# Kernel tuning notes

Hardware: AMD Instinct MI355X
Metric: run time of the kernel (lower is better)

Reference implementation:

```python
import jax, jax.numpy as jnp
import numpy as np

EMBED_DIM = 1024


def setup_inputs() -> dict:
    key = jax.random.key(0)
    ks = jax.random.split(key, 9)
    d = EMBED_DIM
    s = 1.0 / np.sqrt(d)
    x = jax.random.normal(ks[0], (4, 2048, d), dtype=jnp.float32)
    # nn.Linear weights are [out, in]; we store them transposed for x @ W
    Wq = jax.random.uniform(ks[1], (d, d), jnp.float32, -s, s)
    bq = jax.random.uniform(ks[2], (d,), jnp.float32, -s, s)
    Wk = jax.random.uniform(ks[3], (d, d), jnp.float32, -s, s)
    bk = jax.random.uniform(ks[4], (d,), jnp.float32, -s, s)
    Wv = jax.random.uniform(ks[5], (d, d), jnp.float32, -s, s)
    bv = jax.random.uniform(ks[6], (d,), jnp.float32, -s, s)
    Wo = jax.random.uniform(ks[7], (d, d), jnp.float32, -s, s)
    bo = jax.random.uniform(ks[8], (d,), jnp.float32, -s, s)
    return {"x": x, "Wq": Wq, "bq": bq, "Wk": Wk, "bk": bk,
            "Wv": Wv, "bv": bv, "Wo": Wo, "bo": bo}


def reference(x, Wq, bq, Wk, bk, Wv, bv, Wo, bo):
    b, seq_len, d = x.shape
    scaling = 1.0 / jnp.sqrt(jnp.float32(d))
    q = x @ Wq + bq  # [b, s, d]
    k = x @ Wk + bk
    v = x @ Wv + bv
    scores = jnp.einsum('bqd,bkd->bqk', q, k) * scaling  # [b, s, s]
    causal = jnp.tril(jnp.ones((seq_len, seq_len), dtype=bool))
    scores = jnp.where(causal, scores, -jnp.inf)
    attn = jax.nn.softmax(scores, axis=-1)
    out = jnp.einsum('bqk,bkd->bqd', attn, v)
    return out @ Wo + bo
```

## Files before the change

### kernel.cpp

```cpp
#include <hip/hip_runtime.h>
#include <stdint.h>

typedef __bf16 bf16_t;
typedef __bf16 bf16x8 __attribute__((ext_vector_type(8)));
typedef __bf16 bf16x4 __attribute__((ext_vector_type(4)));
typedef float  f32x4  __attribute__((ext_vector_type(4)));

#define DEV __device__ __forceinline__

constexpr int S = 2048, D = 1024, BATCH = 4, MF = BATCH * S;

DEV void gload16(const void* g, void* l) {
  __builtin_amdgcn_global_load_lds(
      (const __attribute__((address_space(1))) void*)g,
      (__attribute__((address_space(3))) void*)(uint32_t)(uintptr_t)l,
      16, 0, 0);
}

template<int EP>
DEV void gemm_body(int tm, int tn, int bz,
                   const bf16_t* __restrict__ A, const bf16_t* __restrict__ B,
                   void* __restrict__ C0, void* __restrict__ C1,
                   void* __restrict__ C2, const float* __restrict__ aux,
                   float* __restrict__ part, int K, int kmax,
                   bf16_t* ldsA, bf16_t* ldsB)
{
  const int m0 = tm * 128, n0 = tn * 128;
  const int tid  = threadIdx.x;
  const int lane = tid & 63;
  const int wave = tid >> 6;
  const int wm = wave & 1, wn = wave >> 1;
  const int l8r = lane >> 3;
  const int swz = ((lane & 7) ^ (lane >> 3)) * 8;
  const int cl  = lane & 15;
  const int qd  = lane >> 4;
  const int ch0 = ((qd ^ (cl & 7)) * 8);

  f32x4 acc[4][4] = {};

  for (int k0 = 0; k0 < kmax; k0 += 64) {
    #pragma unroll
    for (int t = 0; t < 4; ++t) {
      const int rb = wave * 4 + t;
      gload16(A + (long)(m0 + rb * 8 + l8r) * K + (k0 + swz), &ldsA[rb * 512]);
      gload16(B + (long)(n0 + rb * 8 + l8r) * K + (k0 + swz), &ldsB[rb * 512]);
    }
    __syncthreads();
    #pragma unroll
    for (int kk = 0; kk < 64; kk += 32) {
      bf16x8 af[4], bg[4];
      #pragma unroll
      for (int i = 0; i < 4; ++i)
        af[i] = *(const bf16x8*)&ldsA[(wm * 64 + i * 16 + cl) * 64 + (ch0 ^ kk)];
      #pragma unroll
      for (int j = 0; j < 4; ++j)
        bg[j] = *(const bf16x8*)&ldsB[(wn * 64 + j * 16 + cl) * 64 + (ch0 ^ kk)];
      #pragma unroll
      for (int i = 0; i < 4; ++i)
        #pragma unroll
        for (int j = 0; j < 4; ++j)
          acc[i][j] = __builtin_amdgcn_mfma_f32_16x16x32_bf16(af[i], bg[j], acc[i][j], 0, 0, 0);
    }
    __syncthreads();
  }

  #pragma unroll
  for (int i = 0; i < 4; ++i) {
    const int gm0 = m0 + wm * 64 + i * 16 + qd * 4;

    if (EP == 0) {
      float* Co = (float*)C0;
      #pragma unroll
      for (int j = 0; j < 4; ++j) {
        const int gn = n0 + wn * 64 + j * 16 + cl;
        const float bn = aux[gn];
        #pragma unroll
        for (int r = 0; r < 4; ++r)
          Co[(long)(gm0 + r) * D + gn] = acc[i][j][r] + bn;
      }
    }

    if (EP == 1) {
      bf16_t* q  = (bf16_t*)C0;
      bf16_t* k  = (bf16_t*)C1;
      bf16_t* vT = (bf16_t*)C2;
      #pragma unroll
      for (int j = 0; j < 4; ++j) {
        const int gn  = n0 + wn * 64 + j * 16 + cl;
        const int sec = gn >> 10, ln = gn & 1023;
        const float bn = aux[gn];
        if (sec == 2) {
          const int z = gm0 >> 11, s0 = gm0 & 2047;
          bf16x4 v4;
          #pragma unroll
          for (int r = 0; r < 4; ++r) v4[r] = (bf16_t)(acc[i][j][r] + bn);
          *(bf16x4*)&vT[((long)z * D + ln) * S + s0] = v4;
        } else {
          bf16_t* dst = (sec == 0) ? q : k;
          #pragma unroll
          for (int r = 0; r < 4; ++r)
            dst[(long)(gm0 + r) * D + ln] = (bf16_t)(acc[i][j][r] + bn);
        }
      }
    }

    if (EP == 2) {
      bf16_t* probs = (bf16_t*)C0 + (long)bz * S * S;
      float ls[4] = {0.f, 0.f, 0.f, 0.f};
      #pragma unroll
      for (int j = 0; j < 4; ++j) {
        const int gn = n0 + wn * 64 + j * 16 + cl;
        #pragma unroll
        for (int r = 0; r < 4; ++r) {
          const int gm = gm0 + r;
          const float e = (gn <= gm) ? __expf(acc[i][j][r] * 0.03125f) : 0.0f;
          probs[(long)gm * S + gn] = (bf16_t)e;
          ls[r] += e;
        }
      }
      #pragma unroll
      for (int r = 0; r < 4; ++r) {
        float v = ls[r];
        v += __shfl_xor(v, 1); v += __shfl_xor(v, 2);
        v += __shfl_xor(v, 4); v += __shfl_xor(v, 8);
        if (cl == 0)
          part[((long)bz * S + (gm0 + r)) * 32 + tn * 2 + wn] = v;
      }
    }

    if (EP == 3) {
      bf16_t* attn = (bf16_t*)C0 + (long)bz * S * D;
      const float* invl = aux + (long)bz * S;
      float scl[4];
      #pragma unroll
      for (int r = 0; r < 4; ++r) scl[r] = invl[gm0 + r];
      #pragma unroll
      for (int j = 0; j < 4; ++j) {
        const int gn = n0 + wn * 64 + j * 16 + cl;
        #pragma unroll
        for (int r = 0; r < 4; ++r)
          attn[(long)(gm0 + r) * D + gn] = (bf16_t)(acc[i][j][r] * scl[r]);
      }
    }
  }
}

__global__ __launch_bounds__(256, 4) void gemm_qkv(
    const bf16_t* __restrict__ A, const bf16_t* __restrict__ B,
    bf16_t* q, bf16_t* k, bf16_t* vT, const float* __restrict__ bias)
{
  __shared__ __align__(16) bf16_t lA[128 * 64], lB[128 * 64];
  #pragma unroll
  for (int t = 0; t < 2; ++t) {
    const int l = (int)blockIdx.x + t * 768;
    gemm_body<1>(l & 63, l >> 6, 0, A, B, q, k, vT, bias, nullptr,
                 1024, 1024, lA, lB);
  }
}

__global__ __launch_bounds__(256, 4) void gemm_sc(
    const bf16_t* __restrict__ q, const bf16_t* __restrict__ k,
    bf16_t* probs, float* part)
{
  __shared__ __align__(16) bf16_t lA[128 * 64], lB[128 * 64];
  const int l = blockIdx.x, xcd = l & 7, idx = l >> 3;
  const int bz = xcd >> 1;
  const int t  = (xcd & 1) * 68 + idx;
  int tm = (int)((sqrtf(8.0f * t + 1.0f) - 1.0f) * 0.5f);
  while ((tm + 1) * (tm + 2) / 2 <= t) ++tm;
  while (tm * (tm + 1) / 2 > t) --tm;
  const int tn = t - tm * (tm + 1) / 2;
  gemm_body<2>(tm, tn, bz, q + (long)bz * S * D, k + (long)bz * S * D,
               probs, nullptr, nullptr, nullptr, part, 1024, 1024, lA, lB);
}

__global__ __launch_bounds__(256, 4) void gemm_pv(
    const bf16_t* __restrict__ probs, const bf16_t* __restrict__ vT,
    bf16_t* attn, const float* __restrict__ invl)
{
  __shared__ __align__(16) bf16_t lA[128 * 64], lB[128 * 64];
  const int l = blockIdx.x, xcd = l & 7, idx = l >> 3;
  const int bz = xcd >> 1, half = xcd & 1;
  const int slot = idx >> 3, tn = idx & 7;
  const int tm = (slot & 1) ? (slot - 1 + half) : (15 - half - slot);
  const int kmax = (tm + 1) * 128;
  gemm_body<3>(tm, tn, bz, probs + (long)bz * S * S, vT + (long)bz * D * S,
               attn, nullptr, nullptr, invl, nullptr, 2048, kmax, lA, lB);
}

__global__ __launch_bounds__(256, 4) void gemm_oproj(
    const bf16_t* __restrict__ attn, const bf16_t* __restrict__ WoT,
    float* out, const float* __restrict__ bo)
{
  __shared__ __align__(16) bf16_t lA[128 * 64], lB[128 * 64];
  gemm_body<0>(blockIdx.x, blockIdx.y, 0, attn, WoT, out, nullptr, nullptr,
               bo, nullptr, 1024, 1024, lA, lB);
}

__global__ __launch_bounds__(256) void reduce_invl(
    const float* __restrict__ part, float* __restrict__ invl)
{
  const int r = blockIdx.x * 256 + threadIdx.x;
  const int row = r & (S - 1);
  const int cnt = ((row >> 7) + 1) * 2;
  const float* p = part + (long)r * 32;
  float s = 0.f;
  for (int j = 0; j < cnt; ++j) s += p[j];
  invl[r] = 1.0f / s;
}

__global__ __launch_bounds__(256) void cvt_x(
    const float4* __restrict__ in, bf16x4* __restrict__ out, int n4)
{
  const int i = blockIdx.x * 256 + threadIdx.x;
  if (i >= n4) return;
  float4 f = in[i];
  bf16x4 o;
  o.x = (__bf16)f.x; o.y = (__bf16)f.y; o.z = (__bf16)f.z; o.w = (__bf16)f.w;
  out[i] = o;
}

__global__ __launch_bounds__(256) void cvt_w_t4(
    const float* __restrict__ W0, const float* __restrict__ W1,
    const float* __restrict__ W2, const float* __restrict__ W3,
    bf16_t* __restrict__ dst)
{
  const float* W = (blockIdx.z == 0) ? W0 : (blockIdx.z == 1) ? W1
                 : (blockIdx.z == 2) ? W2 : W3;
  bf16_t* WT = dst + (size_t)blockIdx.z * D * D;
  __shared__ float t[32][33];
  const int bx = blockIdx.x, by = blockIdx.y;
  const int tx = threadIdx.x & 31, ty = threadIdx.x >> 5;
  #pragma unroll
  for (int dy = 0; dy < 32; dy += 8)
    t[ty + dy][tx] = W[(long)(by * 32 + ty + dy) * 1024 + bx * 32 + tx];
  __syncthreads();
  #pragma unroll
  for (int dy = 0; dy < 32; dy += 8)
    WT[(long)(bx * 32 + ty + dy) * 1024 + by * 32 + tx] = (bf16_t)t[tx][ty + dy];
}

__global__ __launch_bounds__(256) void stack_bias(
    const float* __restrict__ bq, const float* __restrict__ bk,
    const float* __restrict__ bv, float* __restrict__ o)
{
  const int i = blockIdx.x * 256 + threadIdx.x;
  const float* s = (i < 1024) ? bq : (i < 2048) ? bk : bv;
  o[i] = s[i & 1023];
}

extern "C" void kernel_launch(void* const* d_in, const int* in_sizes, int n_in,
                              void* d_out, int out_size, void* d_ws, size_t ws_size,
                              hipStream_t stream) {
  const float* x  = (const float*)d_in[0];
  const float* Wq = (const float*)d_in[1];
  const float* bq = (const float*)d_in[2];
  const float* Wk = (const float*)d_in[3];
  const float* bk = (const float*)d_in[4];
  const float* Wv = (const float*)d_in[5];
  const float* bv = (const float*)d_in[6];
  const float* Wo = (const float*)d_in[7];
  const float* bo = (const float*)d_in[8];
  float* out = (float*)d_out;

  size_t off = 0;
  auto alloc = [&](size_t bytes) -> void* {
    void* p = (char*)d_ws + off;
    off += (bytes + 255) & ~(size_t)255;
    return p;
  };
  bf16_t* x_b   = (bf16_t*)alloc((size_t)MF * D * 2);
  bf16_t* Wall  = (bf16_t*)alloc((size_t)4 * D * D * 2);
  float*  bqkv  = (float*) alloc((size_t)3 * D * 4);
  bf16_t* q_b   = (bf16_t*)alloc((size_t)MF * D * 2);
  bf16_t* k_b   = (bf16_t*)alloc((size_t)MF * D * 2);
  bf16_t* vT_b  = (bf16_t*)alloc((size_t)BATCH * D * S * 2);
  bf16_t* probs = (bf16_t*)alloc((size_t)BATCH * S * S * 2);
  float*  part  = (float*) alloc((size_t)MF * 32 * 4);
  float*  invl  = (float*) alloc((size_t)MF * 4);
  bf16_t* attn  = (bf16_t*)alloc((size_t)MF * D * 2);
  bf16_t* WqkvT = Wall;
  bf16_t* WoT   = Wall + (size_t)3 * D * D;

  cvt_x<<<dim3((MF * D / 4 + 255) / 256), 256, 0, stream>>>(
      (const float4*)x, (bf16x4*)x_b, MF * D / 4);
  cvt_w_t4<<<dim3(32, 32, 4), 256, 0, stream>>>(Wq, Wk, Wv, Wo, Wall);
  stack_bias<<<dim3(12), 256, 0, stream>>>(bq, bk, bv, bqkv);

  gemm_qkv<<<dim3(768), 256, 0, stream>>>(x_b, WqkvT, q_b, k_b, vT_b, bqkv);

  gemm_sc<<<dim3(544), 256, 0, stream>>>(q_b, k_b, probs, part);

  reduce_invl<<<dim3(MF / 256), 256, 0, stream>>>(part, invl);

  gemm_pv<<<dim3(512), 256, 0, stream>>>(probs, vT_b, attn, invl);

  gemm_oproj<<<dim3(64, 8), 256, 0, stream>>>(attn, WoT, out, bo);
}
```

Measured before the change: 251.7 us.

## Fold output projection into value weights to drop separate O-proj GEMM

Precomputes Wv·Wo as a fused bf16 weight (a small 1024x1024 GEMM) and folds the V bias through Wo, so the QKV GEMM directly produces V·Wo. The PV GEMM then writes the final fp32 output with the softmax normalisation and bias, which removes the full-size output-projection GEMM and the attn intermediate buffer. The cost is an extra weight-product GEMM and a serial per-column dot product for the bias. The weight product is rounded to bf16, which slightly changes numerics. The QKV launch also moves from a persistent two-tile loop to a 2D grid.

```diff
diff --git a/kernel.cpp b/kernel.cpp
--- a/kernel.cpp
+++ b/kernel.cpp
@@ -68,22 +68,10 @@
   for (int i = 0; i < 4; ++i) {
     const int gm0 = m0 + wm * 64 + i * 16 + qd * 4;
 
-    if (EP == 0) {
-      float* Co = (float*)C0;
-      #pragma unroll
-      for (int j = 0; j < 4; ++j) {
-        const int gn = n0 + wn * 64 + j * 16 + cl;
-        const float bn = aux[gn];
-        #pragma unroll
-        for (int r = 0; r < 4; ++r)
-          Co[(long)(gm0 + r) * D + gn] = acc[i][j][r] + bn;
-      }
-    }
-
     if (EP == 1) {
       bf16_t* q  = (bf16_t*)C0;
       bf16_t* k  = (bf16_t*)C1;
-      bf16_t* vT = (bf16_t*)C2;
+      bf16_t* vwT = (bf16_t*)C2;
       #pragma unroll
       for (int j = 0; j < 4; ++j) {
         const int gn  = n0 + wn * 64 + j * 16 + cl;
@@ -94,7 +82,7 @@
           bf16x4 v4;
           #pragma unroll
           for (int r = 0; r < 4; ++r) v4[r] = (bf16_t)(acc[i][j][r] + bn);
-          *(bf16x4*)&vT[((long)z * D + ln) * S + s0] = v4;
+          *(bf16x4*)&vwT[((long)z * D + ln) * S + s0] = v4;
         } else {
           bf16_t* dst = (sec == 0) ? q : k;
           #pragma unroll
@@ -129,17 +117,30 @@
     }
 
     if (EP == 3) {
-      bf16_t* attn = (bf16_t*)C0 + (long)bz * S * D;
+      float* out = (float*)C0 + (long)bz * S * D;
       const float* invl = aux + (long)bz * S;
+      const float* bo = (const float*)C1;
       float scl[4];
       #pragma unroll
       for (int r = 0; r < 4; ++r) scl[r] = invl[gm0 + r];
+      #pragma unroll
+      for (int j = 0; j < 4; ++j) {
+        const int gn = n0 + wn * 64 + j * 16 + cl;
+        const float bn = bo[gn];
+        #pragma unroll
+        for (int r = 0; r < 4; ++r)
+          out[(long)(gm0 + r) * D + gn] = acc[i][j][r] * scl[r] + bn;
+      }
+    }
+
+    if (EP == 4) {
+      bf16_t* Co = (bf16_t*)C0;
       #pragma unroll
       for (int j = 0; j < 4; ++j) {
         const int gn = n0 + wn * 64 + j * 16 + cl;
         #pragma unroll
         for (int r = 0; r < 4; ++r)
-          attn[(long)(gm0 + r) * D + gn] = (bf16_t)(acc[i][j][r] * scl[r]);
+          Co[(long)(gm0 + r) * D + gn] = (bf16_t)acc[i][j][r];
       }
     }
   }
@@ -147,15 +148,11 @@
 
 __global__ __launch_bounds__(256, 4) void gemm_qkv(
     const bf16_t* __restrict__ A, const bf16_t* __restrict__ B,
-    bf16_t* q, bf16_t* k, bf16_t* vT, const float* __restrict__ bias)
+    bf16_t* q, bf16_t* k, bf16_t* vwT, const float* __restrict__ bias)
 {
   __shared__ __align__(16) bf16_t lA[128 * 64], lB[128 * 64];
-  #pragma unroll
-  for (int t = 0; t < 2; ++t) {
-    const int l = (int)blockIdx.x + t * 768;
-    gemm_body<1>(l & 63, l >> 6, 0, A, B, q, k, vT, bias, nullptr,
-                 1024, 1024, lA, lB);
-  }
+  gemm_body<1>(blockIdx.x, blockIdx.y, 0, A, B, q, k, vwT, bias, nullptr,
+               1024, 1024, lA, lB);
 }
 
 __global__ __launch_bounds__(256, 4) void gemm_sc(
@@ -174,9 +171,9 @@
                probs, nullptr, nullptr, nullptr, part, 1024, 1024, lA, lB);
 }
 
-__global__ __launch_bounds__(256, 4) void gemm_pv(
-    const bf16_t* __restrict__ probs, const bf16_t* __restrict__ vT,
-    bf16_t* attn, const float* __restrict__ invl)
+__global__ __launch_bounds__(256, 4) void gemm_pv_out(
+    const bf16_t* __restrict__ probs, const bf16_t* __restrict__ vwT,
+    float* out, const float* __restrict__ invl, const float* __restrict__ bo)
 {
   __shared__ __align__(16) bf16_t lA[128 * 64], lB[128 * 64];
   const int l = blockIdx.x, xcd = l & 7, idx = l >> 3;
@@ -184,17 +181,17 @@
   const int slot = idx >> 3, tn = idx & 7;
   const int tm = (slot & 1) ? (slot - 1 + half) : (15 - half - slot);
   const int kmax = (tm + 1) * 128;
-  gemm_body<3>(tm, tn, bz, probs + (long)bz * S * S, vT + (long)bz * D * S,
-               attn, nullptr, nullptr, invl, nullptr, 2048, kmax, lA, lB);
-}
-
-__global__ __launch_bounds__(256, 4) void gemm_oproj(
-    const bf16_t* __restrict__ attn, const bf16_t* __restrict__ WoT,
-    float* out, const float* __restrict__ bo)
+  gemm_body<3>(tm, tn, bz, probs + (long)bz * S * S, vwT + (long)bz * D * S,
+               out, (void*)bo, nullptr, invl, nullptr, 2048, kmax, lA, lB);
+}
+
+__global__ __launch_bounds__(256, 4) void gemm_wvo(
+    const bf16_t* __restrict__ WoT, const bf16_t* __restrict__ WvN,
+    bf16_t* WvoT)
 {
   __shared__ __align__(16) bf16_t lA[128 * 64], lB[128 * 64];
-  gemm_body<0>(blockIdx.x, blockIdx.y, 0, attn, WoT, out, nullptr, nullptr,
-               bo, nullptr, 1024, 1024, lA, lB);
+  gemm_body<4>(blockIdx.x, blockIdx.y, 0, WoT, WvN, WvoT, nullptr, nullptr,
+               nullptr, nullptr, 1024, 1024, lA, lB);
 }
 
 __global__ __launch_bounds__(256) void reduce_invl(
@@ -225,12 +222,23 @@
     const float* __restrict__ W2, const float* __restrict__ W3,
     bf16_t* __restrict__ dst)
 {
+  const int zmap[4] = {0, 1, 3, 4};
   const float* W = (blockIdx.z == 0) ? W0 : (blockIdx.z == 1) ? W1
                  : (blockIdx.z == 2) ? W2 : W3;
-  bf16_t* WT = dst + (size_t)blockIdx.z * D * D;
-  __shared__ float t[32][33];
+  bf16_t* WT = dst + (size_t)zmap[blockIdx.z] * D * D;
   const int bx = blockIdx.x, by = blockIdx.y;
   const int tx = threadIdx.x & 31, ty = threadIdx.x >> 5;
+
+  if (blockIdx.z == 2) {
+    #pragma unroll
+    for (int dy = 0; dy < 32; dy += 8) {
+      const long idx = (long)(by * 32 + ty + dy) * 1024 + bx * 32 + tx;
+      WT[idx] = (bf16_t)W[idx];
+    }
+    return;
+  }
+
+  __shared__ float t[32][33];
   #pragma unroll
   for (int dy = 0; dy < 32; dy += 8)
     t[ty + dy][tx] = W[(long)(by * 32 + ty + dy) * 1024 + bx * 32 + tx];
@@ -242,11 +250,18 @@
 
 __global__ __launch_bounds__(256) void stack_bias(
     const float* __restrict__ bq, const float* __restrict__ bk,
-    const float* __restrict__ bv, float* __restrict__ o)
+    const float* __restrict__ bv, const float* __restrict__ Wo,
+    float* __restrict__ o)
 {
   const int i = blockIdx.x * 256 + threadIdx.x;
-  const float* s = (i < 1024) ? bq : (i < 2048) ? bk : bv;
-  o[i] = s[i & 1023];
+  if (i < 2048) {
+    o[i] = (i < 1024) ? bq[i] : bk[i & 1023];
+  } else {
+    const int c = i - 2048;
+    float s = 0.f;
+    for (int e = 0; e < 1024; ++e) s += bv[e] * Wo[e * 1024 + c];
+    o[i] = s;
+  }
 }
 
 extern "C" void kernel_launch(void* const* d_in, const int* in_sizes, int n_in,
@@ -270,30 +285,31 @@
     return p;
   };
   bf16_t* x_b   = (bf16_t*)alloc((size_t)MF * D * 2);
-  bf16_t* Wall  = (bf16_t*)alloc((size_t)4 * D * D * 2);
+  bf16_t* Wall  = (bf16_t*)alloc((size_t)5 * D * D * 2);
   float*  bqkv  = (float*) alloc((size_t)3 * D * 4);
   bf16_t* q_b   = (bf16_t*)alloc((size_t)MF * D * 2);
   bf16_t* k_b   = (bf16_t*)alloc((size_t)MF * D * 2);
-  bf16_t* vT_b  = (bf16_t*)alloc((size_t)BATCH * D * S * 2);
+  bf16_t* vwT_b = (bf16_t*)alloc((size_t)BATCH * D * S * 2);
   bf16_t* probs = (bf16_t*)alloc((size_t)BATCH * S * S * 2);
   float*  part  = (float*) alloc((size_t)MF * 32 * 4);
   float*  invl  = (float*) alloc((size_t)MF * 4);
-  bf16_t* attn  = (bf16_t*)alloc((size_t)MF * D * 2);
   bf16_t* WqkvT = Wall;
-  bf16_t* WoT   = Wall + (size_t)3 * D * D;
+  bf16_t* WvoT  = Wall + (size_t)2 * D * D;
+  bf16_t* WvN   = Wall + (size_t)3 * D * D;
+  bf16_t* WoT   = Wall + (size_t)4 * D * D;
 
   cvt_x<<<dim3((MF * D / 4 + 255) / 256), 256, 0, stream>>>(
       (const float4*)x, (bf16x4*)x_b, MF * D / 4);
   cvt_w_t4<<<dim3(32, 32, 4), 256, 0, stream>>>(Wq, Wk, Wv, Wo, Wall);
-  stack_bias<<<dim3(12), 256, 0, stream>>>(bq, bk, bv, bqkv);
-
-  gemm_qkv<<<dim3(768), 256, 0, stream>>>(x_b, WqkvT, q_b, k_b, vT_b, bqkv);
+  stack_bias<<<dim3(12), 256, 0, stream>>>(bq, bk, bv, Wo, bqkv);
+
+  gemm_wvo<<<dim3(8, 8), 256, 0, stream>>>(WoT, WvN, WvoT);
+
+  gemm_qkv<<<dim3(64, 24), 256, 0, stream>>>(x_b, WqkvT, q_b, k_b, vwT_b, bqkv);
 
   gemm_sc<<<dim3(544), 256, 0, stream>>>(q_b, k_b, probs, part);
 
   reduce_invl<<<dim3(MF / 256), 256, 0, stream>>>(part, invl);
 
-  gemm_pv<<<dim3(512), 256, 0, stream>>>(probs, vT_b, attn, invl);
-
-  gemm_oproj<<<dim3(64, 8), 256, 0, stream>>>(attn, WoT, out, bo);
-}
+  gemm_pv_out<<<dim3(512), 256, 0, stream>>>(probs, vwT_b, out, invl, bo);
+}
```

Measured after the change: 303.7 us. 1.21x slower.
